# Performance work log

Measured on AMD Instinct MI355X. Metric: run time of the kernel, lower is better.

Reference implementation:

```python
import jax, jax.numpy as jnp
import numpy as np

N_NODES = 100000


def setup_inputs() -> dict:
    key = jax.random.key(0)
    ks = jax.random.split(key, 6)
    x = jax.random.normal(ks[0], (N_NODES, 3), dtype=jnp.float32)
    edge_index = jax.random.randint(ks[1], (2, 1600000), 0, N_NODES, dtype=jnp.int32)
    W1 = jax.random.normal(ks[2], (6, 64), dtype=jnp.float32) * 0.2
    b1 = jnp.zeros((64,), dtype=jnp.float32)
    W2 = jax.random.normal(ks[3], (67, 128), dtype=jnp.float32) * 0.1
    b2 = jnp.zeros((128,), dtype=jnp.float32)
    Wc = jax.random.normal(ks[4], (128, 5), dtype=jnp.float32) * 0.1
    bc = jnp.zeros((5,), dtype=jnp.float32)
    return {"x": x, "edge_index": edge_index, "W1": W1, "b1": b1,
            "W2": W2, "b2": b2, "Wc": Wc, "bc": bc}


def _pointnet_conv(h, rel, src, dst, W, b, n):
    # gather neighbor features, MLP on [h_j, pos_j - pos_i], max-aggregate per node
    msg = jnp.concatenate([h[src], rel], axis=-1) @ W + b  # [E, out]
    agg = jax.ops.segment_max(msg, dst, num_segments=n)    # [N, out]
    return jax.nn.relu(agg)  # relu also maps -inf (isolated nodes) to 0


def reference(x, edge_index, W1, b1, W2, b2, Wc, bc):
    src, dst = edge_index[0], edge_index[1]
    pos = x  # forward uses data.x for both x and pos
    rel = pos[src] - pos[dst]                       # [E, 3]
    h = _pointnet_conv(x, rel, src, dst, W1, b1, N_NODES)   # [N, 64]
    h = _pointnet_conv(h, rel, src, dst, W2, b2, N_NODES)   # [N, 128]
    logits = h @ Wc + bc                            # [N, 5]
    return jax.nn.log_softmax(logits, axis=-1)
```

## Files before the change

kernel.cpp:

```cpp
#include <hip/hip_runtime.h>
#include <cstdint>

#define CAP 56
#define NBITS 8
#define BINSZ 256
#define BIN_CAP 5120
#define TILE_E 8192
#define SCANN 512

typedef _Float16 h2 __attribute__((ext_vector_type(2)));
typedef _Float16 h4 __attribute__((ext_vector_type(4)));
typedef _Float16 h8 __attribute__((ext_vector_type(8)));
typedef float f32x4 __attribute__((ext_vector_type(4)));

static __device__ inline h8 pkmax8(h8 a, h8 b) {
#if __has_builtin(__builtin_elementwise_max)
    return __builtin_elementwise_max(a, b);
#else
    h8 r;
    #pragma unroll
    for (int i = 0; i < 8; i += 2) {
        h2 aa = { a[i], a[i+1] }, bb = { b[i], b[i+1] }, rr;
        asm("v_pk_max_f16 %0, %1, %2" : "=v"(rr) : "v"(aa), "v"(bb));
        r[i] = rr.x; r[i+1] = rr.y;
    }
    return r;
#endif
}

__global__ __launch_bounds__(256) void bin_kernel(
    const int* __restrict__ ei, int* __restrict__ bin_cnt,
    int* __restrict__ pairs, int E, int nbins)
{
    __shared__ int hist[SCANN];
    __shared__ int sc[SCANN];
    __shared__ int gbase[SCANN];
    __shared__ int lofs[SCANN];
    __shared__ int words[TILE_E];
    __shared__ unsigned short binOf[TILE_E];
    int t = threadIdx.x;
    for (int i = t; i < SCANN; i += 256) { hist[i] = 0; lofs[i] = 0; }
    __syncthreads();
    int e0 = blockIdx.x * TILE_E;
    int s[32], d[32];
    #pragma unroll
    for (int i = 0; i < 32; ++i) {
        int e = e0 + t + i * 256;
        bool ok = e < E;
        s[i] = ok ? ei[e] : 0;
        d[i] = ok ? ei[E + e] : -1;
        if (ok) atomicAdd(&hist[d[i] >> NBITS], 1);
    }
    __syncthreads();
    sc[t] = hist[t]; sc[t + 256] = hist[t + 256];
    __syncthreads();
    for (int off = 1; off < SCANN; off <<= 1) {
        int i0 = t, i1 = t + 256;
        int v0 = (i0 >= off) ? sc[i0 - off] : 0;
        int v1 = (i1 >= off) ? sc[i1 - off] : 0;
        __syncthreads();
        sc[i0] += v0; sc[i1] += v1;
        __syncthreads();
    }
    for (int i = t; i < nbins; i += 256)
        gbase[i] = atomicAdd(&bin_cnt[i], hist[i]);
    __syncthreads();
    #pragma unroll
    for (int i = 0; i < 32; ++i) {
        if (d[i] >= 0) {
            int b = d[i] >> NBITS;
            int p = atomicAdd(&lofs[b], 1);
            int slot = (sc[b] - hist[b]) + p;
            words[slot] = s[i] | ((d[i] & (BINSZ - 1)) << 17);
            binOf[slot] = (unsigned short)b;
        }
    }
    __syncthreads();
    int total = sc[nbins - 1];
    for (int i = t; i < total; i += 256) {
        int b = binOf[i];
        int off = gbase[b] + (i - (sc[b] - hist[b]));
        if (off < BIN_CAP) pairs[b * BIN_CAP + off] = words[i];
    }
}

__global__ __launch_bounds__(256) void scatter2_kernel(
    const int* __restrict__ pairs, const int* __restrict__ bin_cnt,
    int* __restrict__ cursor, int* __restrict__ bucket, int N)
{
    __shared__ int cur[BINSZ];
    __shared__ int lbuck[BINSZ * CAP];
    int t = threadIdx.x;
    int b = blockIdx.x;
    for (int i = t; i < BINSZ; i += 256) cur[i] = 0;
    __syncthreads();
    int cnt = min(bin_cnt[b], BIN_CAP);
    const int* pp = pairs + b * BIN_CAP;
    for (int i = t; i < cnt; i += 256) {
        int w = pp[i];
        int p = atomicAdd(&cur[w >> 17], 1);
        if (p < CAP) lbuck[(w >> 17) * CAP + p] = w & 0x1FFFF;
    }
    __syncthreads();
    int nbase = b * BINSZ;
    for (int dl = t; dl < BINSZ; dl += 256) {
        int n = nbase + dl;
        if (n >= N) continue;
        int c = min(cur[dl], CAP);
        int e = (c + 7) & ~7;
        int s0 = (c > 0) ? lbuck[dl * CAP] : 0;
        for (int p = c; p < e; ++p) lbuck[dl * CAP + p] = s0;
        cursor[n] = c;
    }
    __syncthreads();
    int4* dst = (int4*)(bucket + (size_t)nbase * CAP);
    const int4* srcv = (const int4*)lbuck;
    for (int i = t; i < BINSZ * CAP / 4; i += 256) dst[i] = srcv[i];
}

__global__ __launch_bounds__(256) void xpack_kernel(
    const float* __restrict__ x, float4* __restrict__ xp,
    int* __restrict__ bin_cnt, int N)
{
    int n = blockIdx.x * 256 + threadIdx.x;
    if (n < N) xp[n] = make_float4(x[n*3], x[n*3+1], x[n*3+2], 0.f);
    if (blockIdx.x == 0) {
        bin_cnt[threadIdx.x] = 0;
        bin_cnt[threadIdx.x + 256] = 0;
    }
}

__global__ __launch_bounds__(256) void agg1_gemm_kernel(
    const float4* __restrict__ xp, const int* __restrict__ cursor,
    const int* __restrict__ bucket, const float* __restrict__ W1,
    const float* __restrict__ b1, const float* __restrict__ W2,
    const float* __restrict__ b2, _Float16* __restrict__ u2h, int N)
{
    __shared__ _Float16 h1[64 * 72];
    __shared__ _Float16 w2t[128 * 72];
    int tid = threadIdx.x;
    int n0  = blockIdx.x * 64;
    int sub = tid & 15;
    int ng  = tid >> 4;

    {
        const float4* W2v4 = (const float4*)W2;
        #pragma unroll
        for (int it = 0; it < 8; ++it) {
            int idx = tid + it * 256;
            int k   = idx >> 5;
            int c   = (idx & 31) * 4;
            float4 w = W2v4[idx];
            w2t[(c+0)*72 + k] = (_Float16)w.x;
            w2t[(c+1)*72 + k] = (_Float16)w.y;
            w2t[(c+2)*72 + k] = (_Float16)w.z;
            w2t[(c+3)*72 + k] = (_Float16)w.w;
        }
    }

    float4 q0 = ((const float4*)(W1 + 0*64))[sub];
    float4 q1 = ((const float4*)(W1 + 1*64))[sub];
    float4 q2 = ((const float4*)(W1 + 2*64))[sub];
    float4 t0 = ((const float4*)(W1 + 3*64))[sub];
    float4 t1 = ((const float4*)(W1 + 4*64))[sub];
    float4 t2 = ((const float4*)(W1 + 5*64))[sub];
    float4 c0 = make_float4(q0.x+t0.x, q0.y+t0.y, q0.z+t0.z, q0.w+t0.w);
    float4 c1 = make_float4(q1.x+t1.x, q1.y+t1.y, q1.z+t1.z, q1.w+t1.w);
    float4 c2 = make_float4(q2.x+t2.x, q2.y+t2.y, q2.z+t2.z, q2.w+t2.w);
    float4 bb = ((const float4*)b1)[sub];

    #pragma unroll
    for (int pass = 0; pass < 4; ++pass) {
        int nl = pass * 16 + ng;
        int n  = n0 + nl;
        float4 m = make_float4(-3e38f, -3e38f, -3e38f, -3e38f);
        int cnt = 0;
        if (n < N) {
            cnt = cursor[n];
            int rounds = (cnt + 7) & ~7;
            const int4* brow4 = (const int4*)(bucket + (size_t)n * CAP);
            int4 ia = brow4[0], ib = brow4[1];
            for (int j0 = 0; j0 < rounds; j0 += 8) {
                int4 na = brow4[(j0 >> 2) + 2];
                int4 nb = brow4[(j0 >> 2) + 3];
                float4 xs[8];
                xs[0] = xp[ia.x]; xs[1] = xp[ia.y]; xs[2] = xp[ia.z]; xs[3] = xp[ia.w];
                xs[4] = xp[ib.x]; xs[5] = xp[ib.y]; xs[6] = xp[ib.z]; xs[7] = xp[ib.w];
                #pragma unroll
                for (int u = 0; u < 8; ++u) {
                    float4 v;
                    v.x = fmaf(xs[u].x, c0.x, fmaf(xs[u].y, c1.x, xs[u].z * c2.x));
                    v.y = fmaf(xs[u].x, c0.y, fmaf(xs[u].y, c1.y, xs[u].z * c2.y));
                    v.z = fmaf(xs[u].x, c0.z, fmaf(xs[u].y, c1.z, xs[u].z * c2.z));
                    v.w = fmaf(xs[u].x, c0.w, fmaf(xs[u].y, c1.w, xs[u].z * c2.w));
                    m.x = fmaxf(m.x, v.x); m.y = fmaxf(m.y, v.y);
                    m.z = fmaxf(m.z, v.z); m.w = fmaxf(m.w, v.w);
                }
                ia = na; ib = nb;
            }
        }
        float4 xd = (n < N) ? xp[n] : make_float4(0.f, 0.f, 0.f, 0.f);
        float v0 = (cnt > 0) ? fmaxf(m.x + bb.x - (xd.x*t0.x + xd.y*t1.x + xd.z*t2.x), 0.f) : 0.f;
        float v1 = (cnt > 0) ? fmaxf(m.y + bb.y - (xd.x*t0.y + xd.y*t1.y + xd.z*t2.y), 0.f) : 0.f;
        float v2 = (cnt > 0) ? fmaxf(m.z + bb.z - (xd.x*t0.z + xd.y*t1.z + xd.z*t2.z), 0.f) : 0.f;
        float v3 = (cnt > 0) ? fmaxf(m.w + bb.w - (xd.x*t0.w + xd.y*t1.w + xd.z*t2.w), 0.f) : 0.f;
        h4 hv;
        hv.x = (_Float16)v0; hv.y = (_Float16)v1;
        hv.z = (_Float16)v2; hv.w = (_Float16)v3;
        *(h4*)&h1[nl * 72 + 4 * sub] = hv;
    }
    __syncthreads();

    int l   = tid & 63;
    int wv  = tid >> 6;
    int r16 = l & 15;
    int g4  = l >> 4;

    f32x4 acc[8];
    #pragma unroll
    for (int ct = 0; ct < 8; ++ct) acc[ct] = (f32x4){0.f, 0.f, 0.f, 0.f};

    h8 a0 = *(const h8*)&h1[(16*wv + r16) * 72 +      8*g4];
    h8 a1 = *(const h8*)&h1[(16*wv + r16) * 72 + 32 + 8*g4];
    #pragma unroll
    for (int ct = 0; ct < 8; ++ct) {
        h8 b0 = *(const h8*)&w2t[(16*ct + r16) * 72 +      8*g4];
        h8 b1f = *(const h8*)&w2t[(16*ct + r16) * 72 + 32 + 8*g4];
        acc[ct] = __builtin_amdgcn_mfma_f32_16x16x32_f16(a0, b0,  acc[ct], 0, 0, 0);
        acc[ct] = __builtin_amdgcn_mfma_f32_16x16x32_f16(a1, b1f, acc[ct], 0, 0, 0);
    }

    float bbv[8], wxv[8], wyv[8], wzv[8];
    #pragma unroll
    for (int ct = 0; ct < 8; ++ct) {
        int col = 16*ct + r16;
        bbv[ct] = b2[col];
        wxv[ct] = W2[64*128 + col];
        wyv[ct] = W2[65*128 + col];
        wzv[ct] = W2[66*128 + col];
    }
    #pragma unroll
    for (int r = 0; r < 4; ++r) {
        int n = n0 + 16*wv + 4*g4 + r;
        if (n < N) {
            float4 xd = xp[n];
            _Float16* orow = u2h + (size_t)n * 128 + r16;
            #pragma unroll
            for (int ct = 0; ct < 8; ++ct) {
                float v = acc[ct][r] + bbv[ct]
                        + xd.x * wxv[ct] + xd.y * wyv[ct] + xd.z * wzv[ct];
                orow[16*ct] = (_Float16)v;
            }
        }
    }
}

__global__ __launch_bounds__(256) void agg2_head_kernel(
    const float* __restrict__ x, const int* __restrict__ cursor,
    const int* __restrict__ bucket, const float* __restrict__ W2,
    const h8* __restrict__ u2v, const float* __restrict__ Wc,
    const float* __restrict__ bc, float* __restrict__ out, int N)
{
    int gid = blockIdx.x * 256 + threadIdx.x;
    int n   = gid >> 4;
    int sub = threadIdx.x & 15;
    if (n >= N) return;
    int cnt = cursor[n];
    int rounds = (cnt + 7) & ~7;
    const int4* brow4 = (const int4*)(bucket + (size_t)n * CAP);
    const _Float16 NEG = (_Float16)(-60000.0f);
    h8 hm = { NEG, NEG, NEG, NEG, NEG, NEG, NEG, NEG };
    int4 ia = brow4[0], ib = brow4[1];
    for (int j0 = 0; j0 < rounds; j0 += 8) {
        int4 na = brow4[(j0 >> 2) + 2];
        int4 nb = brow4[(j0 >> 2) + 3];
        h8 v0 = u2v[(size_t)ia.x * 16 + sub];
        h8 v1 = u2v[(size_t)ia.y * 16 + sub];
        h8 v2 = u2v[(size_t)ia.z * 16 + sub];
        h8 v3 = u2v[(size_t)ia.w * 16 + sub];
        h8 v4 = u2v[(size_t)ib.x * 16 + sub];
        h8 v5 = u2v[(size_t)ib.y * 16 + sub];
        h8 v6 = u2v[(size_t)ib.z * 16 + sub];
        h8 v7 = u2v[(size_t)ib.w * 16 + sub];
        hm = pkmax8(hm, v0); hm = pkmax8(hm, v1);
        hm = pkmax8(hm, v2); hm = pkmax8(hm, v3);
        hm = pkmax8(hm, v4); hm = pkmax8(hm, v5);
        hm = pkmax8(hm, v6); hm = pkmax8(hm, v7);
        ia = na; ib = nb;
    }
    const float4* W2v = (const float4*)W2;
    float4 wa0 = W2v[64*32 + sub*2], wa1 = W2v[64*32 + sub*2 + 1];
    float4 wb0 = W2v[65*32 + sub*2], wb1 = W2v[65*32 + sub*2 + 1];
    float4 wc0 = W2v[66*32 + sub*2], wc1 = W2v[66*32 + sub*2 + 1];
    float x0 = x[n*3], x1 = x[n*3+1], x2 = x[n*3+2];
    float hh[8];
    hh[0] = (cnt > 0) ? fmaxf((float)hm[0] - (x0*wa0.x + x1*wb0.x + x2*wc0.x), 0.f) : 0.f;
    hh[1] = (cnt > 0) ? fmaxf((float)hm[1] - (x0*wa0.y + x1*wb0.y + x2*wc0.y), 0.f) : 0.f;
    hh[2] = (cnt > 0) ? fmaxf((float)hm[2] - (x0*wa0.z + x1*wb0.z + x2*wc0.z), 0.f) : 0.f;
    hh[3] = (cnt > 0) ? fmaxf((float)hm[3] - (x0*wa0.w + x1*wb0.w + x2*wc0.w), 0.f) : 0.f;
    hh[4] = (cnt > 0) ? fmaxf((float)hm[4] - (x0*wa1.x + x1*wb1.x + x2*wc1.x), 0.f) : 0.f;
    hh[5] = (cnt > 0) ? fmaxf((float)hm[5] - (x0*wa1.y + x1*wb1.y + x2*wc1.y), 0.f) : 0.f;
    hh[6] = (cnt > 0) ? fmaxf((float)hm[6] - (x0*wa1.z + x1*wb1.z + x2*wc1.z), 0.f) : 0.f;
    hh[7] = (cnt > 0) ? fmaxf((float)hm[7] - (x0*wa1.w + x1*wb1.w + x2*wc1.w), 0.f) : 0.f;

    int g = sub * 8;
    float l0 = 0.f, l1 = 0.f, l2 = 0.f, l3 = 0.f, l4 = 0.f;
    #pragma unroll
    for (int k = 0; k < 8; ++k) {
        l0 = fmaf(hh[k], Wc[(g+k)*5+0], l0);
        l1 = fmaf(hh[k], Wc[(g+k)*5+1], l1);
        l2 = fmaf(hh[k], Wc[(g+k)*5+2], l2);
        l3 = fmaf(hh[k], Wc[(g+k)*5+3], l3);
        l4 = fmaf(hh[k], Wc[(g+k)*5+4], l4);
    }
    #pragma unroll
    for (int off = 8; off > 0; off >>= 1) {
        l0 += __shfl_xor(l0, off);
        l1 += __shfl_xor(l1, off);
        l2 += __shfl_xor(l2, off);
        l3 += __shfl_xor(l3, off);
        l4 += __shfl_xor(l4, off);
    }
    l0 += bc[0]; l1 += bc[1]; l2 += bc[2]; l3 += bc[3]; l4 += bc[4];
    float mx  = fmaxf(fmaxf(fmaxf(l0, l1), fmaxf(l2, l3)), l4);
    float s   = expf(l0-mx) + expf(l1-mx) + expf(l2-mx) + expf(l3-mx) + expf(l4-mx);
    float lse = mx + logf(s);
    if (sub < 5) {
        float v = (sub == 0) ? l0 : (sub == 1) ? l1 : (sub == 2) ? l2
                : (sub == 3) ? l3 : l4;
        out[n*5 + sub] = v - lse;
    }
}

extern "C" void kernel_launch(void* const* d_in, const int* in_sizes, int n_in,
                              void* d_out, int out_size, void* d_ws, size_t ws_size,
                              hipStream_t stream)
{
    const float* x  = (const float*)d_in[0];
    const int*   ei = (const int*)d_in[1];
    const float* W1 = (const float*)d_in[2];
    const float* b1 = (const float*)d_in[3];
    const float* W2 = (const float*)d_in[4];
    const float* b2 = (const float*)d_in[5];
    const float* Wc = (const float*)d_in[6];
    const float* bc = (const float*)d_in[7];
    float* out = (float*)d_out;

    int N = in_sizes[0] / 3;
    int E = in_sizes[1] / 2;
    int nbins = (N + BINSZ - 1) / BINSZ;

    char* ws = (char*)d_ws;
    _Float16* u2h   = (_Float16*)(ws);
    float4* xp      = (float4*)(ws + 25600000);
    int*    pairs   = (int*)   (ws + 27200000);
    int*    bucket  = (int*)   (ws + 35250000);
    int*    cursor  = (int*)   (ws + 57700000);
    int*    bin_cnt = (int*)   (ws + 58200000);

    xpack_kernel<<<(N + 255) / 256, 256, 0, stream>>>(x, xp, bin_cnt, N);
    bin_kernel<<<(E + TILE_E - 1) / TILE_E, 256, 0, stream>>>(
        ei, bin_cnt, pairs, E, nbins);
    scatter2_kernel<<<nbins, 256, 0, stream>>>(pairs, bin_cnt, cursor, bucket, N);

    agg1_gemm_kernel<<<(N + 63) / 64, 256, 0, stream>>>(
        xp, cursor, bucket, W1, b1, W2, b2, u2h, N);
    agg2_head_kernel<<<(N * 16 + 255) / 256, 256, 0, stream>>>(
        x, cursor, bucket, W2, (const h8*)u2h, Wc, bc, out, N);
}
```

Baseline: 216.8 us.

## Replace binned two-pass edge sort with direct global-atomic bucket scatter

Drops the shared-memory binning kernel and the per-bin scatter kernel. Edges are now placed straight into per-node buckets using global atomicAdd on a per-node cursor, and a separate pad kernel clamps each count and pads every bucket to a multiple of 8. This removes the intermediate pairs buffer, a kernel launch and the in-block scan, at the cost of about 1.6M random global atomics and uncoalesced writes. The agg2 gather loop is also software-pipelined, so the next round's feature loads are issued before the current round's max reductions.

```diff
diff --git a/kernel.cpp b/kernel.cpp
--- a/kernel.cpp
+++ b/kernel.cpp
@@ -2,11 +2,6 @@
 #include <cstdint>
 
 #define CAP 56
-#define NBITS 8
-#define BINSZ 256
-#define BIN_CAP 5120
-#define TILE_E 8192
-#define SCANN 512
 
 typedef _Float16 h2 __attribute__((ext_vector_type(2)));
 typedef _Float16 h4 __attribute__((ext_vector_type(4)));
@@ -28,105 +23,51 @@
 #endif
 }
 
-__global__ __launch_bounds__(256) void bin_kernel(
-    const int* __restrict__ ei, int* __restrict__ bin_cnt,
-    int* __restrict__ pairs, int E, int nbins)
-{
-    __shared__ int hist[SCANN];
-    __shared__ int sc[SCANN];
-    __shared__ int gbase[SCANN];
-    __shared__ int lofs[SCANN];
-    __shared__ int words[TILE_E];
-    __shared__ unsigned short binOf[TILE_E];
-    int t = threadIdx.x;
-    for (int i = t; i < SCANN; i += 256) { hist[i] = 0; lofs[i] = 0; }
-    __syncthreads();
-    int e0 = blockIdx.x * TILE_E;
-    int s[32], d[32];
-    #pragma unroll
-    for (int i = 0; i < 32; ++i) {
-        int e = e0 + t + i * 256;
-        bool ok = e < E;
-        s[i] = ok ? ei[e] : 0;
-        d[i] = ok ? ei[E + e] : -1;
-        if (ok) atomicAdd(&hist[d[i] >> NBITS], 1);
-    }
-    __syncthreads();
-    sc[t] = hist[t]; sc[t + 256] = hist[t + 256];
-    __syncthreads();
-    for (int off = 1; off < SCANN; off <<= 1) {
-        int i0 = t, i1 = t + 256;
-        int v0 = (i0 >= off) ? sc[i0 - off] : 0;
-        int v1 = (i1 >= off) ? sc[i1 - off] : 0;
-        __syncthreads();
-        sc[i0] += v0; sc[i1] += v1;
-        __syncthreads();
-    }
-    for (int i = t; i < nbins; i += 256)
-        gbase[i] = atomicAdd(&bin_cnt[i], hist[i]);
-    __syncthreads();
-    #pragma unroll
-    for (int i = 0; i < 32; ++i) {
-        if (d[i] >= 0) {
-            int b = d[i] >> NBITS;
-            int p = atomicAdd(&lofs[b], 1);
-            int slot = (sc[b] - hist[b]) + p;
-            words[slot] = s[i] | ((d[i] & (BINSZ - 1)) << 17);
-            binOf[slot] = (unsigned short)b;
-        }
-    }
-    __syncthreads();
-    int total = sc[nbins - 1];
-    for (int i = t; i < total; i += 256) {
-        int b = binOf[i];
-        int off = gbase[b] + (i - (sc[b] - hist[b]));
-        if (off < BIN_CAP) pairs[b * BIN_CAP + off] = words[i];
-    }
-}
-
-__global__ __launch_bounds__(256) void scatter2_kernel(
-    const int* __restrict__ pairs, const int* __restrict__ bin_cnt,
-    int* __restrict__ cursor, int* __restrict__ bucket, int N)
-{
-    __shared__ int cur[BINSZ];
-    __shared__ int lbuck[BINSZ * CAP];
-    int t = threadIdx.x;
-    int b = blockIdx.x;
-    for (int i = t; i < BINSZ; i += 256) cur[i] = 0;
-    __syncthreads();
-    int cnt = min(bin_cnt[b], BIN_CAP);
-    const int* pp = pairs + b * BIN_CAP;
-    for (int i = t; i < cnt; i += 256) {
-        int w = pp[i];
-        int p = atomicAdd(&cur[w >> 17], 1);
-        if (p < CAP) lbuck[(w >> 17) * CAP + p] = w & 0x1FFFF;
-    }
-    __syncthreads();
-    int nbase = b * BINSZ;
-    for (int dl = t; dl < BINSZ; dl += 256) {
-        int n = nbase + dl;
-        if (n >= N) continue;
-        int c = min(cur[dl], CAP);
-        int e = (c + 7) & ~7;
-        int s0 = (c > 0) ? lbuck[dl * CAP] : 0;
-        for (int p = c; p < e; ++p) lbuck[dl * CAP + p] = s0;
-        cursor[n] = c;
-    }
-    __syncthreads();
-    int4* dst = (int4*)(bucket + (size_t)nbase * CAP);
-    const int4* srcv = (const int4*)lbuck;
-    for (int i = t; i < BINSZ * CAP / 4; i += 256) dst[i] = srcv[i];
-}
-
 __global__ __launch_bounds__(256) void xpack_kernel(
     const float* __restrict__ x, float4* __restrict__ xp,
-    int* __restrict__ bin_cnt, int N)
+    int* __restrict__ cursor, int N)
 {
     int n = blockIdx.x * 256 + threadIdx.x;
-    if (n < N) xp[n] = make_float4(x[n*3], x[n*3+1], x[n*3+2], 0.f);
-    if (blockIdx.x == 0) {
-        bin_cnt[threadIdx.x] = 0;
-        bin_cnt[threadIdx.x + 256] = 0;
+    if (n < N) {
+        xp[n] = make_float4(x[n*3], x[n*3+1], x[n*3+2], 0.f);
+        cursor[n] = 0;
+    }
+}
+
+__global__ __launch_bounds__(256) void scatter_kernel(
+    const int* __restrict__ ei, int* __restrict__ cursor,
+    int* __restrict__ bucket, int E)
+{
+    int base = (blockIdx.x * 256 + threadIdx.x) * 4;
+    if (base >= E) return;
+    if (base + 4 <= E) {
+        int4 s4 = *(const int4*)(ei + base);
+        int4 d4 = *(const int4*)(ei + E + base);
+        int p;
+        p = atomicAdd(&cursor[d4.x], 1); if (p < CAP) bucket[(size_t)d4.x * CAP + p] = s4.x;
+        p = atomicAdd(&cursor[d4.y], 1); if (p < CAP) bucket[(size_t)d4.y * CAP + p] = s4.y;
+        p = atomicAdd(&cursor[d4.z], 1); if (p < CAP) bucket[(size_t)d4.z * CAP + p] = s4.z;
+        p = atomicAdd(&cursor[d4.w], 1); if (p < CAP) bucket[(size_t)d4.w * CAP + p] = s4.w;
+    } else {
+        for (int e = base; e < E; ++e) {
+            int s = ei[e], d = ei[E + e];
+            int p = atomicAdd(&cursor[d], 1);
+            if (p < CAP) bucket[(size_t)d * CAP + p] = s;
+        }
+    }
+}
+
+__global__ __launch_bounds__(256) void pad_kernel(
+    int* __restrict__ cursor, int* __restrict__ bucket, int N)
+{
+    int n = blockIdx.x * 256 + threadIdx.x;
+    if (n >= N) return;
+    int c = cursor[n];
+    if (c > CAP) { c = CAP; cursor[n] = CAP; }
+    int e = (c + 7) & ~7;
+    if (c > 0) {
+        int s0 = bucket[(size_t)n * CAP];
+        for (int p = c; p < e; ++p) bucket[(size_t)n * CAP + p] = s0;
     }
 }
 
@@ -266,14 +207,12 @@
     int sub = threadIdx.x & 15;
     if (n >= N) return;
     int cnt = cursor[n];
-    int rounds = (cnt + 7) & ~7;
+    int nr = (cnt + 7) >> 3;
     const int4* brow4 = (const int4*)(bucket + (size_t)n * CAP);
     const _Float16 NEG = (_Float16)(-60000.0f);
     h8 hm = { NEG, NEG, NEG, NEG, NEG, NEG, NEG, NEG };
-    int4 ia = brow4[0], ib = brow4[1];
-    for (int j0 = 0; j0 < rounds; j0 += 8) {
-        int4 na = brow4[(j0 >> 2) + 2];
-        int4 nb = brow4[(j0 >> 2) + 3];
+    if (nr > 0) {
+        int4 ia = brow4[0], ib = brow4[1];
         h8 v0 = u2v[(size_t)ia.x * 16 + sub];
         h8 v1 = u2v[(size_t)ia.y * 16 + sub];
         h8 v2 = u2v[(size_t)ia.z * 16 + sub];
@@ -282,11 +221,29 @@
         h8 v5 = u2v[(size_t)ib.y * 16 + sub];
         h8 v6 = u2v[(size_t)ib.z * 16 + sub];
         h8 v7 = u2v[(size_t)ib.w * 16 + sub];
+        int4 na = brow4[2], nb = brow4[3];
+        #pragma unroll 2
+        for (int r = 1; r < nr; ++r) {
+            h8 w0 = u2v[(size_t)na.x * 16 + sub];
+            h8 w1 = u2v[(size_t)na.y * 16 + sub];
+            h8 w2_ = u2v[(size_t)na.z * 16 + sub];
+            h8 w3 = u2v[(size_t)na.w * 16 + sub];
+            h8 w4 = u2v[(size_t)nb.x * 16 + sub];
+            h8 w5 = u2v[(size_t)nb.y * 16 + sub];
+            h8 w6 = u2v[(size_t)nb.z * 16 + sub];
+            h8 w7 = u2v[(size_t)nb.w * 16 + sub];
+            na = brow4[2*r + 2]; nb = brow4[2*r + 3];
+            hm = pkmax8(hm, v0); hm = pkmax8(hm, v1);
+            hm = pkmax8(hm, v2); hm = pkmax8(hm, v3);
+            hm = pkmax8(hm, v4); hm = pkmax8(hm, v5);
+            hm = pkmax8(hm, v6); hm = pkmax8(hm, v7);
+            v0 = w0; v1 = w1; v2 = w2_; v3 = w3;
+            v4 = w4; v5 = w5; v6 = w6; v7 = w7;
+        }
         hm = pkmax8(hm, v0); hm = pkmax8(hm, v1);
         hm = pkmax8(hm, v2); hm = pkmax8(hm, v3);
         hm = pkmax8(hm, v4); hm = pkmax8(hm, v5);
         hm = pkmax8(hm, v6); hm = pkmax8(hm, v7);
-        ia = na; ib = nb;
     }
     const float4* W2v = (const float4*)W2;
     float4 wa0 = W2v[64*32 + sub*2], wa1 = W2v[64*32 + sub*2 + 1];
@@ -348,20 +305,16 @@
 
     int N = in_sizes[0] / 3;
     int E = in_sizes[1] / 2;
-    int nbins = (N + BINSZ - 1) / BINSZ;
 
     char* ws = (char*)d_ws;
     _Float16* u2h   = (_Float16*)(ws);
     float4* xp      = (float4*)(ws + 25600000);
-    int*    pairs   = (int*)   (ws + 27200000);
     int*    bucket  = (int*)   (ws + 35250000);
     int*    cursor  = (int*)   (ws + 57700000);
-    int*    bin_cnt = (int*)   (ws + 58200000);
-
-    xpack_kernel<<<(N + 255) / 256, 256, 0, stream>>>(x, xp, bin_cnt, N);
-    bin_kernel<<<(E + TILE_E - 1) / TILE_E, 256, 0, stream>>>(
-        ei, bin_cnt, pairs, E, nbins);
-    scatter2_kernel<<<nbins, 256, 0, stream>>>(pairs, bin_cnt, cursor, bucket, N);
+
+    xpack_kernel<<<(N + 255) / 256, 256, 0, stream>>>(x, xp, cursor, N);
+    scatter_kernel<<<(E / 4 + 255) / 256, 256, 0, stream>>>(ei, cursor, bucket, E);
+    pad_kernel<<<(N + 255) / 256, 256, 0, stream>>>(cursor, bucket, N);
 
     agg1_gemm_kernel<<<(N + 63) / 64, 256, 0, stream>>>(
         xp, cursor, bucket, W1, b1, W2, b2, u2h, N);
```

Result: slower. 312.8 us (+44.3%).

## Shrink bins and tiles for more binning blocks; software-pipeline agg2 gathers

Applied to the files above, without the earlier changes.

Bin width drops from 256 to 128 nodes and the edge tile from 8192 to 4096, which doubles the number of bin_kernel and scatter2_kernel blocks and reduces per-block shared memory and registers. The scan widens to 1024 entries to cover the extra bins, and the workspace offsets move. The agg2 gather loop is restructured so the next round's eight feature loads are issued before the current round's max operations, overlapping memory latency with compute. In exchange this costs more global bin atomics, a wider scan, and higher register pressure in agg2.

```diff
diff --git a/kernel.cpp b/kernel.cpp
--- a/kernel.cpp
+++ b/kernel.cpp
@@ -2,11 +2,12 @@
 #include <cstdint>
 
 #define CAP 56
-#define NBITS 8
-#define BINSZ 256
-#define BIN_CAP 5120
-#define TILE_E 8192
-#define SCANN 512
+#define NBITS 7
+#define BINSZ 128
+#define BIN_CAP 2816
+#define TILE_E 4096
+#define SCANN 1024
+#define EPT (TILE_E/256)
 
 typedef _Float16 h2 __attribute__((ext_vector_type(2)));
 typedef _Float16 h4 __attribute__((ext_vector_type(4)));
@@ -26,6 +27,18 @@
     }
     return r;
 #endif
+}
+
+__global__ __launch_bounds__(256) void xpack_kernel(
+    const float* __restrict__ x, float4* __restrict__ xp,
+    int* __restrict__ bin_cnt, int N)
+{
+    int n = blockIdx.x * 256 + threadIdx.x;
+    if (n < N) xp[n] = make_float4(x[n*3], x[n*3+1], x[n*3+2], 0.f);
+    if (blockIdx.x == 0) {
+        #pragma unroll
+        for (int j = 0; j < 4; ++j) bin_cnt[threadIdx.x + j * 256] = 0;
+    }
 }
 
 __global__ __launch_bounds__(256) void bin_kernel(
@@ -42,9 +55,9 @@
     for (int i = t; i < SCANN; i += 256) { hist[i] = 0; lofs[i] = 0; }
     __syncthreads();
     int e0 = blockIdx.x * TILE_E;
-    int s[32], d[32];
-    #pragma unroll
-    for (int i = 0; i < 32; ++i) {
+    int s[EPT], d[EPT];
+    #pragma unroll
+    for (int i = 0; i < EPT; ++i) {
         int e = e0 + t + i * 256;
         bool ok = e < E;
         s[i] = ok ? ei[e] : 0;
@@ -52,21 +65,25 @@
         if (ok) atomicAdd(&hist[d[i] >> NBITS], 1);
     }
     __syncthreads();
-    sc[t] = hist[t]; sc[t + 256] = hist[t + 256];
+    for (int i = t; i < SCANN; i += 256) sc[i] = hist[i];
     __syncthreads();
     for (int off = 1; off < SCANN; off <<= 1) {
-        int i0 = t, i1 = t + 256;
-        int v0 = (i0 >= off) ? sc[i0 - off] : 0;
-        int v1 = (i1 >= off) ? sc[i1 - off] : 0;
+        int v[4];
+        #pragma unroll
+        for (int j = 0; j < 4; ++j) {
+            int i = t + j * 256;
+            v[j] = (i >= off) ? sc[i - off] : 0;
+        }
         __syncthreads();
-        sc[i0] += v0; sc[i1] += v1;
+        #pragma unroll
+        for (int j = 0; j < 4; ++j) sc[t + j * 256] += v[j];
         __syncthreads();
     }
     for (int i = t; i < nbins; i += 256)
         gbase[i] = atomicAdd(&bin_cnt[i], hist[i]);
     __syncthreads();
     #pragma unroll
-    for (int i = 0; i < 32; ++i) {
+    for (int i = 0; i < EPT; ++i) {
         if (d[i] >= 0) {
             int b = d[i] >> NBITS;
             int p = atomicAdd(&lofs[b], 1);
@@ -76,7 +93,7 @@
         }
     }
     __syncthreads();
-    int total = sc[nbins - 1];
+    int total = sc[SCANN - 1];
     for (int i = t; i < total; i += 256) {
         int b = binOf[i];
         int off = gbase[b] + (i - (sc[b] - hist[b]));
@@ -116,18 +133,6 @@
     int4* dst = (int4*)(bucket + (size_t)nbase * CAP);
     const int4* srcv = (const int4*)lbuck;
     for (int i = t; i < BINSZ * CAP / 4; i += 256) dst[i] = srcv[i];
-}
-
-__global__ __launch_bounds__(256) void xpack_kernel(
-    const float* __restrict__ x, float4* __restrict__ xp,
-    int* __restrict__ bin_cnt, int N)
-{
-    int n = blockIdx.x * 256 + threadIdx.x;
-    if (n < N) xp[n] = make_float4(x[n*3], x[n*3+1], x[n*3+2], 0.f);
-    if (blockIdx.x == 0) {
-        bin_cnt[threadIdx.x] = 0;
-        bin_cnt[threadIdx.x + 256] = 0;
-    }
 }
 
 __global__ __launch_bounds__(256) void agg1_gemm_kernel(
@@ -266,14 +271,12 @@
     int sub = threadIdx.x & 15;
     if (n >= N) return;
     int cnt = cursor[n];
-    int rounds = (cnt + 7) & ~7;
+    int nr = (cnt + 7) >> 3;
     const int4* brow4 = (const int4*)(bucket + (size_t)n * CAP);
     const _Float16 NEG = (_Float16)(-60000.0f);
     h8 hm = { NEG, NEG, NEG, NEG, NEG, NEG, NEG, NEG };
-    int4 ia = brow4[0], ib = brow4[1];
-    for (int j0 = 0; j0 < rounds; j0 += 8) {
-        int4 na = brow4[(j0 >> 2) + 2];
-        int4 nb = brow4[(j0 >> 2) + 3];
+    if (nr > 0) {
+        int4 ia = brow4[0], ib = brow4[1];
         h8 v0 = u2v[(size_t)ia.x * 16 + sub];
         h8 v1 = u2v[(size_t)ia.y * 16 + sub];
         h8 v2 = u2v[(size_t)ia.z * 16 + sub];
@@ -282,11 +285,29 @@
         h8 v5 = u2v[(size_t)ib.y * 16 + sub];
         h8 v6 = u2v[(size_t)ib.z * 16 + sub];
         h8 v7 = u2v[(size_t)ib.w * 16 + sub];
+        int4 na = brow4[2], nb = brow4[3];
+        #pragma unroll 2
+        for (int r = 1; r < nr; ++r) {
+            h8 w0 = u2v[(size_t)na.x * 16 + sub];
+            h8 w1 = u2v[(size_t)na.y * 16 + sub];
+            h8 w2_ = u2v[(size_t)na.z * 16 + sub];
+            h8 w3 = u2v[(size_t)na.w * 16 + sub];
+            h8 w4 = u2v[(size_t)nb.x * 16 + sub];
+            h8 w5 = u2v[(size_t)nb.y * 16 + sub];
+            h8 w6 = u2v[(size_t)nb.z * 16 + sub];
+            h8 w7 = u2v[(size_t)nb.w * 16 + sub];
+            na = brow4[2*r + 2]; nb = brow4[2*r + 3];
+            hm = pkmax8(hm, v0); hm = pkmax8(hm, v1);
+            hm = pkmax8(hm, v2); hm = pkmax8(hm, v3);
+            hm = pkmax8(hm, v4); hm = pkmax8(hm, v5);
+            hm = pkmax8(hm, v6); hm = pkmax8(hm, v7);
+            v0 = w0; v1 = w1; v2 = w2_; v3 = w3;
+            v4 = w4; v5 = w5; v6 = w6; v7 = w7;
+        }
         hm = pkmax8(hm, v0); hm = pkmax8(hm, v1);
         hm = pkmax8(hm, v2); hm = pkmax8(hm, v3);
         hm = pkmax8(hm, v4); hm = pkmax8(hm, v5);
         hm = pkmax8(hm, v6); hm = pkmax8(hm, v7);
-        ia = na; ib = nb;
     }
     const float4* W2v = (const float4*)W2;
     float4 wa0 = W2v[64*32 + sub*2], wa1 = W2v[64*32 + sub*2 + 1];
@@ -354,9 +375,9 @@
     _Float16* u2h   = (_Float16*)(ws);
     float4* xp      = (float4*)(ws + 25600000);
     int*    pairs   = (int*)   (ws + 27200000);
-    int*    bucket  = (int*)   (ws + 35250000);
-    int*    cursor  = (int*)   (ws + 57700000);
-    int*    bin_cnt = (int*)   (ws + 58200000);
+    int*    bucket  = (int*)   (ws + 36100000);
+    int*    cursor  = (int*)   (ws + 58600000);
+    int*    bin_cnt = (int*)   (ws + 59100000);
 
     xpack_kernel<<<(N + 255) / 256, 256, 0, stream>>>(x, xp, bin_cnt, N);
     bin_kernel<<<(E + TILE_E - 1) / TILE_E, 256, 0, stream>>>(
```

New measurement: 216.5 us. About the same (-0.1%).
